# Performance work log

Measured on AMD Instinct MI355X. Metric: run time of the kernel, lower is better.

The kernel has to match this reference:

```python
import jax, jax.numpy as jnp
import numpy as np

D_MODEL = 512
D_STATE = 64
D_INNER = 2 * D_MODEL   # standard Mamba expand=2
D_CONV = 4
DT_RANK = D_MODEL // 16  # 32
LN_EPS = 1e-5


def setup_inputs() -> dict:
    key = jax.random.key(0)
    ks = jax.random.split(key, 12)
    B, L = 2, 1024
    s = 0.02
    return {
        "frames": jax.random.normal(ks[0], (B, L, D_MODEL), jnp.float32),
        "gamma": jnp.ones((D_MODEL,), jnp.float32),
        "beta": jnp.zeros((D_MODEL,), jnp.float32),
        "W_in": jax.random.normal(ks[1], (D_MODEL, 2 * D_INNER), jnp.float32) * s,
        "conv_w": jax.random.normal(ks[2], (D_INNER, D_CONV), jnp.float32) * s,
        "conv_b": jnp.zeros((D_INNER,), jnp.float32),
        "W_x": jax.random.normal(ks[3], (D_INNER, DT_RANK + 2 * D_STATE), jnp.float32) * s,
        "W_dt": jax.random.normal(ks[4], (DT_RANK, D_INNER), jnp.float32) * s,
        "b_dt": jax.random.uniform(ks[5], (D_INNER,), jnp.float32, -4.0, -2.0),
        "A_log": jnp.log(jnp.broadcast_to(jnp.arange(1, D_STATE + 1, dtype=jnp.float32), (D_INNER, D_STATE))),
        "D": jnp.ones((D_INNER,), jnp.float32),
        "W_out": jax.random.normal(ks[6], (D_INNER, D_MODEL), jnp.float32) * s,
    }


def reference(frames, gamma, beta, W_in, conv_w, conv_b, W_x, W_dt, b_dt, A_log, D, W_out):
    B, L, _ = frames.shape
    d_inner = W_in.shape[1] // 2
    d_state = A_log.shape[1]
    dt_rank = W_dt.shape[0]
    d_conv = conv_w.shape[1]

    # LayerNorm
    mu = frames.mean(-1, keepdims=True)
    var = ((frames - mu) ** 2).mean(-1, keepdims=True)
    xn = (frames - mu) * jax.lax.rsqrt(var + LN_EPS) * gamma + beta

    # in_proj -> x, z
    x, z = jnp.split(xn @ W_in, 2, axis=-1)  # each (B, L, d_inner)

    # causal depthwise conv1d along time
    xc = jnp.pad(x.transpose(0, 2, 1), ((0, 0), (0, 0), (d_conv - 1, 0)))  # (B, d_inner, L+pad)
    xconv = jax.lax.conv_general_dilated(
        xc, conv_w[:, None, :], (1,), "VALID", feature_group_count=d_inner)  # (B, d_inner, L)
    x = jax.nn.silu(xconv.transpose(0, 2, 1) + conv_b)  # (B, L, d_inner)

    # input-dependent dt, B, C
    xdb = x @ W_x
    dt, Bm, Cm = jnp.split(xdb, [dt_rank, dt_rank + d_state], axis=-1)
    delta = jax.nn.softplus(dt @ W_dt + b_dt)  # (B, L, d_inner)
    A = -jnp.exp(A_log)                        # (d_inner, d_state)

    # selective scan over time
    def step(h, inp):
        d_t, B_t, C_t, x_t = inp  # (B,d_inner) (B,d_state) (B,d_state) (B,d_inner)
        dA = jnp.exp(d_t[..., None] * A)                       # (B,d_inner,d_state)
        h = h * dA + (d_t * x_t)[..., None] * B_t[:, None, :]  # (B,d_inner,d_state)
        y = jnp.einsum("bds,bs->bd", h, C_t)
        return h, y

    h0 = jnp.zeros((B, d_inner, d_state), frames.dtype)
    xs = (delta.transpose(1, 0, 2), Bm.transpose(1, 0, 2),
          Cm.transpose(1, 0, 2), x.transpose(1, 0, 2))
    _, ys = jax.lax.scan(step, h0, xs)  # (L, B, d_inner)

    y = ys.transpose(1, 0, 2) + x * D
    y = y * jax.nn.silu(z)
    return y @ W_out + frames  # residual connection
```

## Files before the change

### kernel.cpp

```cpp
#include <hip/hip_runtime.h>
#include <hip/hip_bf16.h>
#include <math.h>

constexpr int Bn     = 2;
constexpr int Lseq   = 1024;
constexpr int DM     = 512;
constexpr int DI     = 1024;
constexpr int DS     = 64;
constexpr int RNK    = 32;
constexpr int NROWS  = Bn * Lseq;
constexpr int XDBW   = RNK + 2 * DS;
constexpr int CH     = 64;
constexpr int NC     = Lseq / CH;

typedef __attribute__((ext_vector_type(4))) float floatx4;
typedef __attribute__((ext_vector_type(8))) short shortx8;

__device__ __forceinline__ float silu_f(float v) {
    return v / (1.f + __expf(-v));
}

__device__ __forceinline__ float rdl(float v, int l) {
    return __int_as_float(__builtin_amdgcn_readlane(__float_as_int(v), l));
}

__device__ __forceinline__ float bf2f(unsigned short u) {
    return __uint_as_float((unsigned)u << 16);
}

__global__ void ln_kernel(const float* __restrict__ x, const float* __restrict__ g,
                          const float* __restrict__ be, __hip_bfloat16* __restrict__ xn) {
    int row = blockIdx.x;
    int tid = threadIdx.x;
    const float* xr = x + (size_t)row * DM;
    float v0 = xr[tid], v1 = xr[tid + 256];
    float s = v0 + v1, sq = v0 * v0 + v1 * v1;
    #pragma unroll
    for (int o = 1; o < 64; o <<= 1) {
        s  += __shfl_xor(s, o);
        sq += __shfl_xor(sq, o);
    }
    __shared__ float red[8];
    int w = tid >> 6;
    if ((tid & 63) == 0) { red[w] = s; red[4 + w] = sq; }
    __syncthreads();
    float ts = red[0] + red[1] + red[2] + red[3];
    float tq = red[4] + red[5] + red[6] + red[7];
    float mu  = ts * (1.f / DM);
    float var = tq * (1.f / DM) - mu * mu;
    float inv = rsqrtf(var + 1e-5f);
    __hip_bfloat16* o0 = xn + (size_t)row * DM;
    o0[tid]       = __float2bfloat16((v0 - mu) * inv * g[tid]       + be[tid]);
    o0[tid + 256] = __float2bfloat16((v1 - mu) * inv * g[tid + 256] + be[tid + 256]);
}

__global__ void transpose_cast3(const float* __restrict__ Wi, const float* __restrict__ Wo,
                                const float* __restrict__ Wx,
                                __hip_bfloat16* __restrict__ Ti, __hip_bfloat16* __restrict__ To,
                                __hip_bfloat16* __restrict__ Tx) {
    __shared__ float tile[64][65];
    int bid = blockIdx.x;
    const float* in; __hip_bfloat16* out; int R, Cc, bx, by;
    if (bid < 256)      { in = Wi; out = Ti; R = DM; Cc = 2 * DI; bx = bid & 31;        by = bid >> 5; }
    else if (bid < 384) { int b2 = bid - 256; in = Wo; out = To; R = DI; Cc = DM;   bx = b2 & 7;  by = b2 >> 3; }
    else                { int b2 = bid - 384; in = Wx; out = Tx; R = DI; Cc = XDBW; bx = b2 % 3;  by = b2 / 3; }
    int r0 = by * 64, c0 = bx * 64;
    int tid = threadIdx.x;
    #pragma unroll
    for (int i = tid; i < 4096; i += 256) {
        int r = i >> 6, c = i & 63;
        tile[r][c] = (r0 + r < R && c0 + c < Cc) ? in[(size_t)(r0 + r) * Cc + c0 + c] : 0.f;
    }
    __syncthreads();
    #pragma unroll
    for (int i = tid; i < 4096; i += 256) {
        int c = i >> 6, r = i & 63;
        if (r0 + r < R && c0 + c < Cc)
            out[(size_t)(c0 + c) * R + r0 + r] = __float2bfloat16(tile[r][c]);
    }
}

__global__ __launch_bounds__(512) void gemm_inproj(const __hip_bfloat16* __restrict__ A,
                                                   const __hip_bfloat16* __restrict__ Bt,
                                                   __hip_bfloat16* __restrict__ xh,
                                                   __hip_bfloat16* __restrict__ zh,
                                                   int M, int N, int K) {
    __shared__ __hip_bfloat16 As[128 * 32];
    __shared__ __hip_bfloat16 Bs[128 * 32];
    const int tid  = threadIdx.x;
    const int wave = tid >> 6, lane = tid & 63;
    const int m0 = blockIdx.y * 128, n0 = blockIdx.x * 128;
    const int wm = (wave >> 2) * 64, wn = (wave & 3) * 32;

    floatx4 acc[4][2] = {};

    const int arow16 = lane & 15;
    const int kgrp   = lane >> 4;

    for (int k0 = 0; k0 < K; k0 += 32) {
        {
            int i   = tid;
            int row = i >> 2, seg = i & 3;
            const __hip_bfloat16* gA = A  + (size_t)(m0 + row) * K + k0 + seg * 8;
            const __hip_bfloat16* gB = Bt + (size_t)(n0 + row) * K + k0 + seg * 8;
            __hip_bfloat16* lA = As + (size_t)(wave * 64) * 8;
            __hip_bfloat16* lB = Bs + (size_t)(wave * 64) * 8;
            __builtin_amdgcn_global_load_lds(
                (const __attribute__((address_space(1))) void*)gA,
                (__attribute__((address_space(3))) void*)lA, 16, 0, 0);
            __builtin_amdgcn_global_load_lds(
                (const __attribute__((address_space(1))) void*)gB,
                (__attribute__((address_space(3))) void*)lB, 16, 0, 0);
        }
        __syncthreads();

        const shortx8* Asv = (const shortx8*)As;
        const shortx8* Bsv = (const shortx8*)Bs;
        shortx8 a[4], b[2];
        #pragma unroll
        for (int i = 0; i < 4; ++i)
            a[i] = Asv[(wm + i * 16 + arow16) * 4 + kgrp];
        #pragma unroll
        for (int j = 0; j < 2; ++j)
            b[j] = Bsv[(wn + j * 16 + arow16) * 4 + kgrp];
        #pragma unroll
        for (int i = 0; i < 4; ++i)
            #pragma unroll
            for (int j = 0; j < 2; ++j)
                acc[i][j] = __builtin_amdgcn_mfma_f32_16x16x32_bf16(a[i], b[j], acc[i][j], 0, 0, 0);
        __syncthreads();
    }

    const int drow = (lane >> 4) * 4;
    const int dcol = lane & 15;
    const bool isz = (n0 >= DI);
    __hip_bfloat16* dst = isz ? zh : xh;
    const int coloff = isz ? DI : 0;
    #pragma unroll
    for (int i = 0; i < 4; ++i)
        #pragma unroll
        for (int j = 0; j < 2; ++j) {
            int rowb = m0 + wm + i * 16 + drow;
            int col  = n0 + wn + j * 16 + dcol - coloff;
            #pragma unroll
            for (int r = 0; r < 4; ++r)
                dst[(size_t)(rowb + r) * DI + col] = __float2bfloat16(acc[i][j][r]);
        }
}

template<bool RES>
__global__ __launch_bounds__(512) void gemm64_sk(const __hip_bfloat16* __restrict__ A,
                                                 const __hip_bfloat16* __restrict__ Bt,
                                                 const float* __restrict__ Res,
                                                 float* __restrict__ C,
                                                 int M, int N, int K) {
    __shared__ __hip_bfloat16 As[2][64 * 32];
    __shared__ __hip_bfloat16 Bs[2][64 * 32];
    __shared__ float red[256 * 17];
    const int tid  = threadIdx.x;
    const int wave = tid >> 6, lane = tid & 63;
    const int g = wave >> 2, w2 = wave & 3;
    const int m0 = blockIdx.y * 64, n0 = blockIdx.x * 64;
    const int wm = (w2 >> 1) * 32, wn = (w2 & 1) * 32;

    floatx4 acc[2][2] = {};

    const int arow16 = lane & 15;
    const int kgrp   = lane >> 4;
    const int kbeg   = g * (K / 2);

    for (int kk = 0; kk < K / 2; kk += 32) {
        int k0 = kbeg + kk;
        {
            int i   = w2 * 64 + lane;
            int row = i >> 2, seg = i & 3;
            int brow = n0 + row; if (brow >= N) brow = N - 1;
            const __hip_bfloat16* gA = A  + (size_t)(m0 + row) * K + k0 + seg * 8;
            const __hip_bfloat16* gB = Bt + (size_t)brow * K + k0 + seg * 8;
            __hip_bfloat16* lA = As[g] + (size_t)(w2 * 64) * 8;
            __hip_bfloat16* lB = Bs[g] + (size_t)(w2 * 64) * 8;
            __builtin_amdgcn_global_load_lds(
                (const __attribute__((address_space(1))) void*)gA,
                (__attribute__((address_space(3))) void*)lA, 16, 0, 0);
            __builtin_amdgcn_global_load_lds(
                (const __attribute__((address_space(1))) void*)gB,
                (__attribute__((address_space(3))) void*)lB, 16, 0, 0);
        }
        __syncthreads();

        const shortx8* Asv = (const shortx8*)As[g];
        const shortx8* Bsv = (const shortx8*)Bs[g];
        shortx8 a[2], b[2];
        #pragma unroll
        for (int i = 0; i < 2; ++i)
            a[i] = Asv[(wm + i * 16 + arow16) * 4 + kgrp];
        #pragma unroll
        for (int j = 0; j < 2; ++j)
            b[j] = Bsv[(wn + j * 16 + arow16) * 4 + kgrp];
        #pragma unroll
        for (int i = 0; i < 2; ++i)
            #pragma unroll
            for (int j = 0; j < 2; ++j)
                acc[i][j] = __builtin_amdgcn_mfma_f32_16x16x32_bf16(a[i], b[j], acc[i][j], 0, 0, 0);
        __syncthreads();
    }

    int rbase = (w2 * 64 + lane) * 17;
    if (g == 1) {
        #pragma unroll
        for (int i = 0; i < 2; ++i)
            #pragma unroll
            for (int j = 0; j < 2; ++j)
                *(float4*)&red[rbase + (i * 2 + j) * 4] =
                    make_float4(acc[i][j][0], acc[i][j][1], acc[i][j][2], acc[i][j][3]);
    }
    __syncthreads();
    if (g == 0) {
        const int drow = (lane >> 4) * 4;
        const int dcol = lane & 15;
        #pragma unroll
        for (int i = 0; i < 2; ++i)
            #pragma unroll
            for (int j = 0; j < 2; ++j) {
                float4 part = *(const float4*)&red[rbase + (i * 2 + j) * 4];
                int rowb = m0 + wm + i * 16 + drow;
                int col  = n0 + wn + j * 16 + dcol;
                if (col < N) {
                    #pragma unroll
                    for (int r = 0; r < 4; ++r) {
                        size_t idx = (size_t)(rowb + r) * N + col;
                        float v = acc[i][j][r] + (&part.x)[r];
                        if (RES) v += Res[idx];
                        C[idx] = v;
                    }
                }
            }
    }
}

__global__ __launch_bounds__(256) void conv_tile(const __hip_bfloat16* __restrict__ xh,
                                                 const __hip_bfloat16* __restrict__ zh,
                                                 const float* __restrict__ cw,
                                                 const float* __restrict__ cb,
                                                 __hip_bfloat16* __restrict__ xcv_bf,
                                                 __hip_bfloat16* __restrict__ xcvT,
                                                 __hip_bfloat16* __restrict__ zgT) {
    __shared__ float xt[67][68];
    __shared__ float tb[64][65];
    __shared__ float tb2[64][65];
    int t0 = blockIdx.x * 64, d0 = blockIdx.y * 64, b = blockIdx.z;
    int tid = threadIdx.x;
    size_t rowbase = (size_t)b * Lseq;

    for (int i = tid; i < 67 * 16; i += 256) {
        int r = i >> 4, j = i & 15;
        int t = t0 - 3 + r;
        float4 v4 = make_float4(0.f, 0.f, 0.f, 0.f);
        if (t >= 0) {
            ushort4 u = *(const ushort4*)&xh[(rowbase + t) * DI + d0 + j * 4];
            v4 = make_float4(bf2f(u.x), bf2f(u.y), bf2f(u.z), bf2f(u.w));
        }
        *(float4*)&xt[r][j * 4] = v4;
    }
    for (int i = tid; i < 64 * 16; i += 256) {
        int r = i >> 4, j = i & 15;
        ushort4 u = *(const ushort4*)&zh[(rowbase + t0 + r) * DI + d0 + j * 4];
        tb2[r][j * 4 + 0] = silu_f(bf2f(u.x));
        tb2[r][j * 4 + 1] = silu_f(bf2f(u.y));
        tb2[r][j * 4 + 2] = silu_f(bf2f(u.z));
        tb2[r][j * 4 + 3] = silu_f(bf2f(u.w));
    }
    __syncthreads();

    {
        int d = tid & 63, tg = tid >> 6;
        float4 cwv = *(const float4*)&cw[(d0 + d) * 4];
        float cbv = cb[d0 + d];
        #pragma unroll
        for (int i = 0; i < 16; ++i) {
            int t = tg * 16 + i;
            float acc = cbv;
            #pragma unroll
            for (int k = 0; k < 4; ++k) acc += xt[t + k][d] * (&cwv.x)[k];
            float v = silu_f(acc);
            tb[t][d] = v;
            xcv_bf[(rowbase + t0 + t) * DI + d0 + d] = __float2bfloat16(v);
        }
    }
    __syncthreads();

    {
        int t2 = tid & 63, dg2 = tid >> 6;
        #pragma unroll
        for (int i = 0; i < 16; ++i) {
            int d = dg2 * 16 + i;
            size_t orow = ((size_t)(b * DI + d0 + d)) * Lseq + t0 + t2;
            xcvT[orow] = __float2bfloat16(tb[t2][d]);
            zgT[orow]  = __float2bfloat16(tb2[t2][d]);
        }
    }
}

__global__ void delta_kernel(const float* __restrict__ xdb, const float* __restrict__ Wdt,
                             const float* __restrict__ bdt, float* __restrict__ delta) {
    int row = blockIdx.y;
    int d = blockIdx.x * 256 + threadIdx.x;
    __shared__ float dtv[RNK];
    if (threadIdx.x < RNK) dtv[threadIdx.x] = xdb[(size_t)row * XDBW + threadIdx.x];
    __syncthreads();
    float acc = bdt[d];
    #pragma unroll
    for (int r = 0; r < RNK; ++r) acc += dtv[r] * Wdt[(size_t)r * DI + d];
    float sp = (acc > 20.f) ? acc : log1pf(__expf(acc));
    delta[(size_t)row * DI + d] = sp;
}

__global__ __launch_bounds__(512) void scan_chunk1(
        const float* __restrict__ delta, const __hip_bfloat16* __restrict__ xcvT,
        const float* __restrict__ xdb, const float* __restrict__ A_log,
        float* __restrict__ hend, float* __restrict__ dsum) {
    __shared__ float Bsh[64][68];
    __shared__ float dsh[8][64];
    __shared__ float xsh[8][64];

    int blk = blockIdx.x;
    int dg  = blk & (DI / 8 - 1);
    int bc  = blk >> 7;
    int c = bc & (NC - 1), b = bc >> 4;
    int tid = threadIdx.x, w = tid >> 6, lane = tid & 63;
    int d = dg * 8 + w;
    int r0 = b * Lseq + c * CH;

    #pragma unroll
    for (int k = 0; k < 2; ++k) {
        int idx = tid + k * 512;
        int row = idx >> 4, j4 = idx & 15;
        float4 v = *(const float4*)&xdb[(size_t)(r0 + row) * XDBW + RNK + j4 * 4];
        *(float4*)&Bsh[row][j4 * 4] = v;
    }
    {
        int t = tid >> 3, ww = tid & 7;
        dsh[ww][t] = delta[(size_t)(r0 + t) * DI + dg * 8 + ww];
        xsh[w][lane] = bf2f(((const unsigned short*)xcvT)[((size_t)(b * DI + d)) * Lseq + c * CH + lane]);
    }
    __syncthreads();

    float a = -__expf(A_log[d * DS + lane]);
    float vd  = dsh[w][lane];
    float vpx = vd * xsh[w][lane];
    float h = 0.f;
    #pragma unroll 16
    for (int t = 0; t < CH; ++t) {
        float dt_ = rdl(vd, t);
        float px  = rdl(vpx, t);
        h = h * __expf(dt_ * a) + px * Bsh[t][lane];
    }
    float S = vd;
    #pragma unroll
    for (int o = 1; o < 64; o <<= 1) S += __shfl_xor(S, o);
    size_t base = ((size_t)bc * DI + d) * 64;
    hend[base + lane] = h;
    if (lane == 0) dsum[(size_t)bc * DI + d] = S;
}

__global__ __launch_bounds__(256) void scan_stitch(
        const float* __restrict__ hend, const float* __restrict__ dsum,
        const float* __restrict__ A_log, float* __restrict__ hstart) {
    int idx = blockIdx.x * 4 + (threadIdx.x >> 6);
    int lane = threadIdx.x & 63;
    int b = idx >> 10, d = idx & (DI - 1);
    float a = -__expf(A_log[d * DS + lane]);
    float h = 0.f;
    #pragma unroll
    for (int c = 0; c < NC; ++c) {
        size_t base = ((size_t)(b * NC + c) * DI + d) * 64;
        hstart[base + lane] = h;
        float he = hend[base + lane];
        float S  = dsum[(size_t)(b * NC + c) * DI + d];
        h = he + __expf(a * S) * h;
    }
}

__global__ __launch_bounds__(512) void scan_chunk2(
        const float* __restrict__ delta, const __hip_bfloat16* __restrict__ xcvT,
        const float* __restrict__ xdb, const __hip_bfloat16* __restrict__ zgT,
        const float* __restrict__ A_log, const float* __restrict__ Dp,
        const float* __restrict__ hstart, __hip_bfloat16* __restrict__ y_row) {
    __shared__ unsigned int BCsh[64][65];
    __shared__ float dsh[8][64];
    __shared__ float xsh[8][64];
    __shared__ float zsh[8][64];
    __shared__ float P[8][8 * 65];

    int blk = blockIdx.x;
    int dg  = blk & (DI / 8 - 1);
    int bc  = blk >> 7;
    int c = bc & (NC - 1), b = bc >> 4;
    int tid = threadIdx.x, w = tid >> 6, lane = tid & 63;
    int d = dg * 8 + w;
    int r0 = b * Lseq + c * CH;

    #pragma unroll
    for (int k = 0; k < 2; ++k) {
        int i = tid + k * 512;
        int t = i >> 4, sg = i & 15;
        const float* rowp = &xdb[(size_t)(r0 + t) * XDBW + RNK];
        float4 bv = *(const float4*)&rowp[sg * 4];
        float4 cv = *(const float4*)&rowp[DS + sg * 4];
        uint4 pk;
        #pragma unroll
        for (int j = 0; j < 4; ++j) {
            unsigned int bb = __float_as_uint((&bv.x)[j]);
            unsigned int cc2 = __float_as_uint((&cv.x)[j]);
            (&pk.x)[j] = (cc2 & 0xFFFF0000u) | (bb >> 16);
        }
        *(uint4*)&BCsh[t][sg * 4] = pk;
    }
    {
        int t = tid >> 3, ww = tid & 7;
        dsh[ww][t] = delta[(size_t)(r0 + t) * DI + dg * 8 + ww];
        size_t trow = ((size_t)(b * DI + d)) * Lseq + c * CH + lane;
        xsh[w][lane] = bf2f(((const unsigned short*)xcvT)[trow]);
        zsh[w][lane] = bf2f(((const unsigned short*)zgT)[trow]);
    }
    __syncthreads();

    float a  = -__expf(A_log[d * DS + lane]);
    float Dv = Dp[d];
    float vd  = dsh[w][lane];
    float vpx = vd * xsh[w][lane];
    float h = hstart[((size_t)bc * DI + d) * 64 + lane];
    float* Pw = P[w];
    float yreg = 0.f;
    const int tr = lane & 7, q = lane >> 3;

    #pragma unroll
    for (int t8 = 0; t8 < 8; ++t8) {
        #pragma unroll
        for (int tt = 0; tt < 8; ++tt) {
            int t = t8 * 8 + tt;
            unsigned int bcp = BCsh[t][lane];
            float Bt = __uint_as_float(bcp << 16);
            float Ct = __uint_as_float(bcp & 0xFFFF0000u);
            float dt_ = rdl(vd, t);
            float px  = rdl(vpx, t);
            h = h * __expf(dt_ * a) + px * Bt;
            Pw[tt * 65 + lane] = h * Ct;
        }
        float sacc = 0.f;
        #pragma unroll
        for (int j = 0; j < 8; ++j) sacc += Pw[tr * 65 + q * 8 + j];
        sacc += __shfl_xor(sacc, 8);
        sacc += __shfl_xor(sacc, 16);
        sacc += __shfl_xor(sacc, 32);
        if (q == t8) yreg = sacc;
    }

    float yv = (yreg + xsh[w][lane] * Dv) * zsh[w][lane];

    __syncthreads();
    float* T = (float*)P;
    T[lane * 9 + w] = yv;
    __syncthreads();
    {
        int t = tid >> 3, dd = tid & 7;
        float v = T[t * 9 + dd];
        y_row[(size_t)(r0 + t) * DI + dg * 8 + dd] = __float2bfloat16(v);
    }
}

extern "C" void kernel_launch(void* const* d_in, const int* in_sizes, int n_in,
                              void* d_out, int out_size, void* d_ws, size_t ws_size,
                              hipStream_t stream) {
    const float* frames = (const float*)d_in[0];
    const float* gamma  = (const float*)d_in[1];
    const float* beta   = (const float*)d_in[2];
    const float* W_in   = (const float*)d_in[3];
    const float* conv_w = (const float*)d_in[4];
    const float* conv_b = (const float*)d_in[5];
    const float* W_x    = (const float*)d_in[6];
    const float* W_dt   = (const float*)d_in[7];
    const float* b_dt   = (const float*)d_in[8];
    const float* A_log  = (const float*)d_in[9];
    const float* Dp     = (const float*)d_in[10];
    const float* W_out  = (const float*)d_in[11];
    float* out = (float*)d_out;

    char* ws = (char*)d_ws;
    __hip_bfloat16* xn_bf  = (__hip_bfloat16*)ws; ws += (size_t)NROWS * DM * 2;
    __hip_bfloat16* Wt_in  = (__hip_bfloat16*)ws; ws += (size_t)(2 * DI) * DM * 2;
    __hip_bfloat16* Wt_out = (__hip_bfloat16*)ws; ws += (size_t)DM * DI * 2;
    __hip_bfloat16* Wt_x   = (__hip_bfloat16*)ws; ws += (size_t)XDBW * DI * 2;
    __hip_bfloat16* y_row  = (__hip_bfloat16*)ws; ws += (size_t)NROWS * DI * 2;
    __hip_bfloat16* xcv_bf = (__hip_bfloat16*)ws; ws += (size_t)NROWS * DI * 2;
    __hip_bfloat16* xh     = (__hip_bfloat16*)ws; ws += (size_t)NROWS * DI * 2;
    __hip_bfloat16* zh     = (__hip_bfloat16*)ws; ws += (size_t)NROWS * DI * 2;
    __hip_bfloat16* xcvT   = (__hip_bfloat16*)ws; ws += (size_t)NROWS * DI * 2;
    __hip_bfloat16* zgT    = (__hip_bfloat16*)ws; ws += (size_t)NROWS * DI * 2;
    float* xdb    = (float*)ws;  ws += (size_t)NROWS * XDBW * 4;
    float* delta  = (float*)ws;  ws += (size_t)NROWS * DI * 4;
    float* hend   = (float*)ws;  ws += (size_t)Bn * NC * DI * 64 * 4;
    float* hstart = (float*)ws;  ws += (size_t)Bn * NC * DI * 64 * 4;
    float* dsum   = (float*)ws;  ws += (size_t)Bn * NC * DI * 4;

    transpose_cast3<<<432, 256, 0, stream>>>(W_in, W_out, W_x, Wt_in, Wt_out, Wt_x);

    ln_kernel<<<NROWS, 256, 0, stream>>>(frames, gamma, beta, xn_bf);

    gemm_inproj<<<dim3(2 * DI / 128, NROWS / 128), 512, 0, stream>>>(
        xn_bf, Wt_in, xh, zh, NROWS, 2 * DI, DM);

    conv_tile<<<dim3(Lseq / 64, DI / 64, Bn), 256, 0, stream>>>(
        xh, zh, conv_w, conv_b, xcv_bf, xcvT, zgT);

    gemm64_sk<false><<<dim3((XDBW + 63) / 64, NROWS / 64), 512, 0, stream>>>(
        xcv_bf, Wt_x, nullptr, xdb, NROWS, XDBW, DI);

    delta_kernel<<<dim3(DI / 256, NROWS), 256, 0, stream>>>(xdb, W_dt, b_dt, delta);

    scan_chunk1<<<Bn * NC * (DI / 8), 512, 0, stream>>>(delta, xcvT, xdb, A_log, hend, dsum);
    scan_stitch<<<Bn * DI / 4, 256, 0, stream>>>(hend, dsum, A_log, hstart);
    scan_chunk2<<<Bn * NC * (DI / 8), 512, 0, stream>>>(delta, xcvT, xdb, zgT, A_log, Dp, hstart, y_row);

    gemm64_sk<true><<<dim3(DM / 64, NROWS / 64), 512, 0, stream>>>(
        y_row, Wt_out, frames, out, NROWS, DM, DI);
}
```

Baseline: 236.3 us.

## Fuse delta computation into scan kernels and merge layernorm with weight transpose

Removes the standalone delta kernel and its 8 MB fp32 intermediate. Each scan kernel now recomputes softplus(dt @ W_dt + b_dt) per lane from xdb. Layernorm and the weight transpose/cast are merged into one launch with block-index dispatch. This saves two launches and the delta write/read traffic, but the delta matmul and softplus are now computed twice, once in each scan pass, with strided W_dt loads per thread.

Result: slower. 256.5 us (+8.5%).

```diff
diff --git a/kernel.cpp b/kernel.cpp
--- a/kernel.cpp
+++ b/kernel.cpp
@@ -28,44 +28,62 @@
     return __uint_as_float((unsigned)u << 16);
 }
 
-__global__ void ln_kernel(const float* __restrict__ x, const float* __restrict__ g,
-                          const float* __restrict__ be, __hip_bfloat16* __restrict__ xn) {
-    int row = blockIdx.x;
+__device__ __forceinline__ float delta_of(const float* __restrict__ xdb, size_t row,
+                                          const float* __restrict__ Wdt,
+                                          const float* __restrict__ bdt, int d) {
+    float acc = bdt[d];
+    const float* dtrow = &xdb[row * XDBW];
+    #pragma unroll
+    for (int r = 0; r < RNK; r += 4) {
+        float4 dtv = *(const float4*)&dtrow[r];
+        acc += dtv.x * Wdt[(size_t)r * DI + d];
+        acc += dtv.y * Wdt[(size_t)(r + 1) * DI + d];
+        acc += dtv.z * Wdt[(size_t)(r + 2) * DI + d];
+        acc += dtv.w * Wdt[(size_t)(r + 3) * DI + d];
+    }
+    return (acc > 20.f) ? acc : log1pf(__expf(acc));
+}
+
+__global__ void prep_kernel(const float* __restrict__ x, const float* __restrict__ g,
+                            const float* __restrict__ be,
+                            const float* __restrict__ Wi, const float* __restrict__ Wo,
+                            const float* __restrict__ Wx,
+                            __hip_bfloat16* __restrict__ xn,
+                            __hip_bfloat16* __restrict__ Ti, __hip_bfloat16* __restrict__ To,
+                            __hip_bfloat16* __restrict__ Tx) {
+    __shared__ float tile[64][65];
+    __shared__ float red[8];
+    int bid = blockIdx.x;
     int tid = threadIdx.x;
-    const float* xr = x + (size_t)row * DM;
-    float v0 = xr[tid], v1 = xr[tid + 256];
-    float s = v0 + v1, sq = v0 * v0 + v1 * v1;
-    #pragma unroll
-    for (int o = 1; o < 64; o <<= 1) {
-        s  += __shfl_xor(s, o);
-        sq += __shfl_xor(sq, o);
-    }
-    __shared__ float red[8];
-    int w = tid >> 6;
-    if ((tid & 63) == 0) { red[w] = s; red[4 + w] = sq; }
-    __syncthreads();
-    float ts = red[0] + red[1] + red[2] + red[3];
-    float tq = red[4] + red[5] + red[6] + red[7];
-    float mu  = ts * (1.f / DM);
-    float var = tq * (1.f / DM) - mu * mu;
-    float inv = rsqrtf(var + 1e-5f);
-    __hip_bfloat16* o0 = xn + (size_t)row * DM;
-    o0[tid]       = __float2bfloat16((v0 - mu) * inv * g[tid]       + be[tid]);
-    o0[tid + 256] = __float2bfloat16((v1 - mu) * inv * g[tid + 256] + be[tid + 256]);
-}
-
-__global__ void transpose_cast3(const float* __restrict__ Wi, const float* __restrict__ Wo,
-                                const float* __restrict__ Wx,
-                                __hip_bfloat16* __restrict__ Ti, __hip_bfloat16* __restrict__ To,
-                                __hip_bfloat16* __restrict__ Tx) {
-    __shared__ float tile[64][65];
-    int bid = blockIdx.x;
+    if (bid < NROWS) {
+        int row = bid;
+        const float* xr = x + (size_t)row * DM;
+        float v0 = xr[tid], v1 = xr[tid + 256];
+        float s = v0 + v1, sq = v0 * v0 + v1 * v1;
+        #pragma unroll
+        for (int o = 1; o < 64; o <<= 1) {
+            s  += __shfl_xor(s, o);
+            sq += __shfl_xor(sq, o);
+        }
+        int w = tid >> 6;
+        if ((tid & 63) == 0) { red[w] = s; red[4 + w] = sq; }
+        __syncthreads();
+        float ts = red[0] + red[1] + red[2] + red[3];
+        float tq = red[4] + red[5] + red[6] + red[7];
+        float mu  = ts * (1.f / DM);
+        float var = tq * (1.f / DM) - mu * mu;
+        float inv = rsqrtf(var + 1e-5f);
+        __hip_bfloat16* o0 = xn + (size_t)row * DM;
+        o0[tid]       = __float2bfloat16((v0 - mu) * inv * g[tid]       + be[tid]);
+        o0[tid + 256] = __float2bfloat16((v1 - mu) * inv * g[tid + 256] + be[tid + 256]);
+        return;
+    }
+    int b2 = bid - NROWS;
     const float* in; __hip_bfloat16* out; int R, Cc, bx, by;
-    if (bid < 256)      { in = Wi; out = Ti; R = DM; Cc = 2 * DI; bx = bid & 31;        by = bid >> 5; }
-    else if (bid < 384) { int b2 = bid - 256; in = Wo; out = To; R = DI; Cc = DM;   bx = b2 & 7;  by = b2 >> 3; }
-    else                { int b2 = bid - 384; in = Wx; out = Tx; R = DI; Cc = XDBW; bx = b2 % 3;  by = b2 / 3; }
+    if (b2 < 256)      { in = Wi; out = Ti; R = DM; Cc = 2 * DI; bx = b2 & 31; by = b2 >> 5; }
+    else if (b2 < 384) { int b3 = b2 - 256; in = Wo; out = To; R = DI; Cc = DM;   bx = b3 & 7; by = b3 >> 3; }
+    else               { int b3 = b2 - 384; in = Wx; out = Tx; R = DI; Cc = XDBW; bx = b3 % 3; by = b3 / 3; }
     int r0 = by * 64, c0 = bx * 64;
-    int tid = threadIdx.x;
     #pragma unroll
     for (int i = tid; i < 4096; i += 256) {
         int r = i >> 6, c = i & 63;
@@ -301,26 +319,12 @@
     }
 }
 
-__global__ void delta_kernel(const float* __restrict__ xdb, const float* __restrict__ Wdt,
-                             const float* __restrict__ bdt, float* __restrict__ delta) {
-    int row = blockIdx.y;
-    int d = blockIdx.x * 256 + threadIdx.x;
-    __shared__ float dtv[RNK];
-    if (threadIdx.x < RNK) dtv[threadIdx.x] = xdb[(size_t)row * XDBW + threadIdx.x];
-    __syncthreads();
-    float acc = bdt[d];
-    #pragma unroll
-    for (int r = 0; r < RNK; ++r) acc += dtv[r] * Wdt[(size_t)r * DI + d];
-    float sp = (acc > 20.f) ? acc : log1pf(__expf(acc));
-    delta[(size_t)row * DI + d] = sp;
-}
-
 __global__ __launch_bounds__(512) void scan_chunk1(
-        const float* __restrict__ delta, const __hip_bfloat16* __restrict__ xcvT,
-        const float* __restrict__ xdb, const float* __restrict__ A_log,
+        const __hip_bfloat16* __restrict__ xcvT, const float* __restrict__ xdb,
+        const float* __restrict__ A_log, const float* __restrict__ Wdt,
+        const float* __restrict__ bdt,
         float* __restrict__ hend, float* __restrict__ dsum) {
     __shared__ float Bsh[64][68];
-    __shared__ float dsh[8][64];
     __shared__ float xsh[8][64];
 
     int blk = blockIdx.x;
@@ -338,16 +342,12 @@
         float4 v = *(const float4*)&xdb[(size_t)(r0 + row) * XDBW + RNK + j4 * 4];
         *(float4*)&Bsh[row][j4 * 4] = v;
     }
-    {
-        int t = tid >> 3, ww = tid & 7;
-        dsh[ww][t] = delta[(size_t)(r0 + t) * DI + dg * 8 + ww];
-        xsh[w][lane] = bf2f(((const unsigned short*)xcvT)[((size_t)(b * DI + d)) * Lseq + c * CH + lane]);
-    }
-    __syncthreads();
-
+    xsh[w][lane] = bf2f(((const unsigned short*)xcvT)[((size_t)(b * DI + d)) * Lseq + c * CH + lane]);
+    __syncthreads();
+
+    float vd  = delta_of(xdb, (size_t)(r0 + lane), Wdt, bdt, d);
+    float vpx = vd * xsh[w][lane];
     float a = -__expf(A_log[d * DS + lane]);
-    float vd  = dsh[w][lane];
-    float vpx = vd * xsh[w][lane];
     float h = 0.f;
     #pragma unroll 16
     for (int t = 0; t < CH; ++t) {
@@ -382,12 +382,12 @@
 }
 
 __global__ __launch_bounds__(512) void scan_chunk2(
-        const float* __restrict__ delta, const __hip_bfloat16* __restrict__ xcvT,
-        const float* __restrict__ xdb, const __hip_bfloat16* __restrict__ zgT,
+        const __hip_bfloat16* __restrict__ xcvT, const float* __restrict__ xdb,
+        const __hip_bfloat16* __restrict__ zgT,
         const float* __restrict__ A_log, const float* __restrict__ Dp,
+        const float* __restrict__ Wdt, const float* __restrict__ bdt,
         const float* __restrict__ hstart, __hip_bfloat16* __restrict__ y_row) {
     __shared__ unsigned int BCsh[64][65];
-    __shared__ float dsh[8][64];
     __shared__ float xsh[8][64];
     __shared__ float zsh[8][64];
     __shared__ float P[8][8 * 65];
@@ -417,18 +417,16 @@
         *(uint4*)&BCsh[t][sg * 4] = pk;
     }
     {
-        int t = tid >> 3, ww = tid & 7;
-        dsh[ww][t] = delta[(size_t)(r0 + t) * DI + dg * 8 + ww];
         size_t trow = ((size_t)(b * DI + d)) * Lseq + c * CH + lane;
         xsh[w][lane] = bf2f(((const unsigned short*)xcvT)[trow]);
         zsh[w][lane] = bf2f(((const unsigned short*)zgT)[trow]);
     }
     __syncthreads();
 
+    float vd  = delta_of(xdb, (size_t)(r0 + lane), Wdt, bdt, d);
+    float vpx = vd * xsh[w][lane];
     float a  = -__expf(A_log[d * DS + lane]);
     float Dv = Dp[d];
-    float vd  = dsh[w][lane];
-    float vpx = vd * xsh[w][lane];
     float h = hstart[((size_t)bc * DI + d) * 64 + lane];
     float* Pw = P[w];
     float yreg = 0.f;
@@ -498,14 +496,12 @@
     __hip_bfloat16* xcvT   = (__hip_bfloat16*)ws; ws += (size_t)NROWS * DI * 2;
     __hip_bfloat16* zgT    = (__hip_bfloat16*)ws; ws += (size_t)NROWS * DI * 2;
     float* xdb    = (float*)ws;  ws += (size_t)NROWS * XDBW * 4;
-    float* delta  = (float*)ws;  ws += (size_t)NROWS * DI * 4;
     float* hend   = (float*)ws;  ws += (size_t)Bn * NC * DI * 64 * 4;
     float* hstart = (float*)ws;  ws += (size_t)Bn * NC * DI * 64 * 4;
     float* dsum   = (float*)ws;  ws += (size_t)Bn * NC * DI * 4;
 
-    transpose_cast3<<<432, 256, 0, stream>>>(W_in, W_out, W_x, Wt_in, Wt_out, Wt_x);
-
-    ln_kernel<<<NROWS, 256, 0, stream>>>(frames, gamma, beta, xn_bf);
+    prep_kernel<<<NROWS + 432, 256, 0, stream>>>(frames, gamma, beta, W_in, W_out, W_x,
+                                                 xn_bf, Wt_in, Wt_out, Wt_x);
 
     gemm_inproj<<<dim3(2 * DI / 128, NROWS / 128), 512, 0, stream>>>(
         xn_bf, Wt_in, xh, zh, NROWS, 2 * DI, DM);
@@ -516,11 +512,10 @@
     gemm64_sk<false><<<dim3((XDBW + 63) / 64, NROWS / 64), 512, 0, stream>>>(
         xcv_bf, Wt_x, nullptr, xdb, NROWS, XDBW, DI);
 
-    delta_kernel<<<dim3(DI / 256, NROWS), 256, 0, stream>>>(xdb, W_dt, b_dt, delta);
-
-    scan_chunk1<<<Bn * NC * (DI / 8), 512, 0, stream>>>(delta, xcvT, xdb, A_log, hend, dsum);
+    scan_chunk1<<<Bn * NC * (DI / 8), 512, 0, stream>>>(xcvT, xdb, A_log, W_dt, b_dt, hend, dsum);
     scan_stitch<<<Bn * DI / 4, 256, 0, stream>>>(hend, dsum, A_log, hstart);
-    scan_chunk2<<<Bn * NC * (DI / 8), 512, 0, stream>>>(delta, xcvT, xdb, zgT, A_log, Dp, hstart, y_row);
+    scan_chunk2<<<Bn * NC * (DI / 8), 512, 0, stream>>>(xcvT, xdb, zgT, A_log, Dp, W_dt, b_dt,
+                                                        hstart, y_row);
 
     gemm64_sk<true><<<dim3(DM / 64, NROWS / 64), 512, 0, stream>>>(
         y_row, Wt_out, frames, out, NROWS, DM, DI);
```
